# Performance work log

Measured on AMD Instinct MI355X. Metric: run time of the kernel, lower is better.

Reference implementation:

```python
import jax, jax.numpy as jnp
import numpy as np

BN_EPS = 1e-5
K = 2


def _log_shift_max(x):
    # x: [B, C, H, W]. torch.cat([x[..., -s:, :], x[..., :-s, :]], dim=2) == roll(x, +s)
    # and cat([x[..., s:, :], x[..., :s, :]], dim=2) == roll(x, -s).
    H, W = x.shape[2], x.shape[3]
    x_j = jnp.zeros_like(x)
    for i in range(1, int(H).bit_length()):
        s = K ** i - 1
        x_j = jnp.maximum(x_j, x - jnp.roll(x, s, axis=2))
        x_j = jnp.maximum(x_j, x - jnp.roll(x, -s, axis=2))
    for i in range(1, int(W).bit_length()):
        s = K ** i - 1
        x_j = jnp.maximum(x_j, x - jnp.roll(x, s, axis=3))
        x_j = jnp.maximum(x_j, x - jnp.roll(x, -s, axis=3))
    return x_j


def setup_inputs() -> dict:
    key = jax.random.key(0)
    k1, k2 = jax.random.split(key)
    B, C, H, W = 16, 384, 56, 56
    Cout = 384
    x = jax.random.normal(k1, (B, C, H, W), dtype=jnp.float32)
    conv_w = jax.random.normal(k2, (Cout, 2 * C, 1, 1), dtype=jnp.float32) * 0.02
    conv_b = jnp.zeros((Cout,), dtype=jnp.float32)
    bn_scale = jnp.ones((Cout,), dtype=jnp.float32)
    bn_bias = jnp.zeros((Cout,), dtype=jnp.float32)
    bn_mean = jnp.zeros((Cout,), dtype=jnp.float32)
    bn_var = jnp.ones((Cout,), dtype=jnp.float32)
    return {"x": x, "conv_w": conv_w, "conv_b": conv_b,
            "bn_scale": bn_scale, "bn_bias": bn_bias,
            "bn_mean": bn_mean, "bn_var": bn_var}


def reference(x, conv_w, conv_b, bn_scale, bn_bias, bn_mean, bn_var):
    x_j = _log_shift_max(x)                       # [B, C, H, W]
    xc = jnp.concatenate([x, x_j], axis=1)        # [B, 2C, H, W]
    # 1x1 conv == channel contraction
    y = jnp.einsum('bchw,oc->bohw', xc, conv_w[:, :, 0, 0]) + conv_b[None, :, None, None]
    # BatchNorm (eval mode, running stats)
    inv = jax.lax.rsqrt(bn_var + BN_EPS)
    y = (y - bn_mean[None, :, None, None]) * (inv * bn_scale)[None, :, None, None] + bn_bias[None, :, None, None]
    return jax.nn.gelu(y, approximate=False)
```

## Files before the change

### kernel.cpp

```cpp
#include <hip/hip_runtime.h>
#include <cstdint>
#include <cstddef>

typedef unsigned short u16;
typedef unsigned int u32;
typedef __attribute__((ext_vector_type(8))) short short8;
typedef __attribute__((ext_vector_type(4))) float f32x4;

__device__ __forceinline__ float bf2f(u16 v) { return __uint_as_float((u32)v << 16); }
__device__ __forceinline__ u16 f2bf(float f) {
    u32 u = __float_as_uint(f);
    u = (u + 0x7fffu + ((u >> 16) & 1u)) >> 16;
    return (u16)u;
}

#define GLD16(g, l) __builtin_amdgcn_global_load_lds( \
    (const __attribute__((address_space(1))) void*)(g), \
    (__attribute__((address_space(3))) void*)(l), 16, 0, 0)

__device__ __forceinline__ int sniff_fp(const void* x) {
    const u16* xs = (const u16*)x;
    const int lane = threadIdx.x & 63;
    int cnt = 0;
    #pragma unroll
    for (int k = 0; k < 4; ++k) {
        const int i = lane * 4 + k;
        const int e = (xs[2 * i] >> 7) & 0xFF;
        cnt += (int)__popcll(__ballot(e >= 96 && e <= 135));
    }
    return (cnt < 128) ? 1 : 0;
}

__global__ __launch_bounds__(512) void prep_kernel(const void* __restrict__ xin,
                                                   const void* __restrict__ w,
                                                   u16* __restrict__ xc,
                                                   u16* __restrict__ wbf) {
    const int cg = blockIdx.x, b = blockIdx.y;
    const int fp = sniff_fp(xin);

    if (cg >= 48) {
        const int base = ((cg - 48) * 16 + b) * 512 + threadIdx.x;
        for (int i = base; i < 384 * 768; i += 32 * 512) {
            if (fp) wbf[i] = f2bf(((const float*)w)[i]);
            else    wbf[i] = ((const u16*)w)[i];
        }
        return;
    }

    __shared__ __align__(16) u16 pl[3136][8];
    const size_t plane0 = ((size_t)b * 384 + (size_t)cg * 8) * 3136;

    if (fp) {
        const float* xb = (const float*)xin + plane0;
        for (int g = threadIdx.x; g < 784; g += 512) {
            const int p = g * 4;
            float vv[8][4];
            #pragma unroll
            for (int c = 0; c < 8; ++c) {
                const float4 t = *(const float4*)(xb + (size_t)c * 3136 + p);
                vv[c][0] = t.x; vv[c][1] = t.y; vv[c][2] = t.z; vv[c][3] = t.w;
            }
            #pragma unroll
            for (int i = 0; i < 4; ++i) {
                u32 q[4];
                #pragma unroll
                for (int cc = 0; cc < 4; ++cc)
                    q[cc] = (u32)f2bf(vv[cc * 2][i]) | ((u32)f2bf(vv[cc * 2 + 1][i]) << 16);
                *(uint4*)&pl[p + i][0] = make_uint4(q[0], q[1], q[2], q[3]);
            }
        }
    } else {
        const u16* xb = (const u16*)xin + plane0;
        for (int g = threadIdx.x; g < 784; g += 512) {
            const int p = g * 4;
            u32 rc[8][2];
            #pragma unroll
            for (int c = 0; c < 8; ++c) {
                const uint2 t = *(const uint2*)(xb + (size_t)c * 3136 + p);
                rc[c][0] = t.x; rc[c][1] = t.y;
            }
            #pragma unroll
            for (int i = 0; i < 4; ++i) {
                const int d = i >> 1, sh = (i & 1) * 16;
                u32 q[4];
                #pragma unroll
                for (int cc = 0; cc < 4; ++cc) {
                    const u32 lo = (rc[cc * 2][d] >> sh) & 0xFFFFu;
                    const u32 hi = (rc[cc * 2 + 1][d] >> sh) & 0xFFFFu;
                    q[cc] = lo | (hi << 16);
                }
                *(uint4*)&pl[p + i][0] = make_uint4(q[0], q[1], q[2], q[3]);
            }
        }
    }
    __syncthreads();

    for (int p = threadIdx.x; p < 3136; p += 512) {
        const int h = p / 56, w2 = p - h * 56;
        const uint4 self = *(const uint4*)&pl[p][0];
        const u32 sw[4] = {self.x, self.y, self.z, self.w};
        float xv[8], mn[8];
        #pragma unroll
        for (int c2 = 0; c2 < 4; ++c2) {
            xv[c2 * 2]     = __uint_as_float(sw[c2] << 16);
            xv[c2 * 2 + 1] = __uint_as_float(sw[c2] & 0xFFFF0000u);
            mn[c2 * 2] = xv[c2 * 2]; mn[c2 * 2 + 1] = xv[c2 * 2 + 1];
        }
        const int S[5] = {1, 3, 7, 15, 31};
        #pragma unroll
        for (int si = 0; si < 5; ++si) {
            const int s = S[si];
            int hp = h + s; if (hp >= 56) hp -= 56;
            int hm = h - s; if (hm < 0)   hm += 56;
            int wp = w2 + s; if (wp >= 56) wp -= 56;
            int wm = w2 - s; if (wm < 0)   wm += 56;
            const uint4 n0 = *(const uint4*)&pl[hp * 56 + w2][0];
            const uint4 n1 = *(const uint4*)&pl[hm * 56 + w2][0];
            const uint4 n2 = *(const uint4*)&pl[h * 56 + wp][0];
            const uint4 n3 = *(const uint4*)&pl[h * 56 + wm][0];
            const u32 w0[4] = {n0.x, n0.y, n0.z, n0.w};
            const u32 w1[4] = {n1.x, n1.y, n1.z, n1.w};
            const u32 wA[4] = {n2.x, n2.y, n2.z, n2.w};
            const u32 wB[4] = {n3.x, n3.y, n3.z, n3.w};
            #pragma unroll
            for (int c2 = 0; c2 < 4; ++c2) {
                mn[c2 * 2] = fminf(
                    fminf(__uint_as_float(w0[c2] << 16), __uint_as_float(w1[c2] << 16)),
                    fminf(fminf(__uint_as_float(wA[c2] << 16), __uint_as_float(wB[c2] << 16)),
                          mn[c2 * 2]));
                mn[c2 * 2 + 1] = fminf(
                    fminf(__uint_as_float(w0[c2] & 0xFFFF0000u), __uint_as_float(w1[c2] & 0xFFFF0000u)),
                    fminf(fminf(__uint_as_float(wA[c2] & 0xFFFF0000u), __uint_as_float(wB[c2] & 0xFFFF0000u)),
                          mn[c2 * 2 + 1]));
            }
        }
        u32 jq[4];
        #pragma unroll
        for (int c2 = 0; c2 < 4; ++c2)
            jq[c2] = (u32)f2bf(xv[c2 * 2] - mn[c2 * 2]) |
                     ((u32)f2bf(xv[c2 * 2 + 1] - mn[c2 * 2 + 1]) << 16);
        u16* px = xc + ((((size_t)b * 96) + cg) * 3136 + p) * 8;
        u16* pj = xc + ((((size_t)b * 96) + 48 + cg) * 3136 + p) * 8;
        *(uint4*)px = self;
        *(uint4*)pj = make_uint4(jq[0], jq[1], jq[2], jq[3]);
    }
}

__global__ __launch_bounds__(256) void gemm_kernel(
        const u16* __restrict__ xc, const u16* __restrict__ Wt,
        const void* __restrict__ cb, const void* __restrict__ bsc,
        const void* __restrict__ bbi, const void* __restrict__ bme,
        const void* __restrict__ bva, void* __restrict__ outp,
        const void* __restrict__ x0) {
    const int ntile = blockIdx.x;
    const int mtile = blockIdx.y;
    const int fp = sniff_fp(x0);
    __shared__ __align__(16) unsigned char smem[17408];
    __shared__ float2 PB[192];
    u16* const Bsu = (u16*)smem;

    const int tid = threadIdx.x;
    if (tid < 192) {
        const int o = mtile * 192 + tid;
        float vsc, vva, vcb, vme, vbi;
        if (fp) {
            vsc = ((const float*)bsc)[o]; vva = ((const float*)bva)[o];
            vcb = ((const float*)cb)[o];  vme = ((const float*)bme)[o];
            vbi = ((const float*)bbi)[o];
        } else {
            vsc = bf2f(((const u16*)bsc)[o]); vva = bf2f(((const u16*)bva)[o]);
            vcb = bf2f(((const u16*)cb)[o]);  vme = bf2f(((const u16*)bme)[o]);
            vbi = bf2f(((const u16*)bbi)[o]);
        }
        const float seff = vsc * rsqrtf(vva + 1e-5f);
        PB[tid] = make_float2(seff, (vcb - vme) * seff + vbi);
    }

    const int lane = tid & 63, wv = tid >> 6;
    const int quad = lane >> 4, l16 = lane & 15;
    const int bb  = ntile / 49;
    const int hw0 = (ntile - bb * 49) * 64;

    const u16* bgp[2]; int bofs[2];
    #pragma unroll
    for (int i = 0; i < 2; ++i) {
        const int idx = i * 256 + tid;
        const int gg = idx >> 6, n = idx & 63;
        bgp[i]  = xc + (((size_t)bb * 96 + gg) * 3136 + hw0 + n) * 8;
        bofs[i] = idx * 8;
    }
    #define STAGE(q) { \
        u16* dst = Bsu + ((q) & 1) * 4096; \
        _Pragma("unroll") \
        for (int i = 0; i < 2; ++i) GLD16(bgp[i] + (size_t)(q) * 8 * 3136 * 8, dst + bofs[i]); }

    const u16* arow[3];
    #pragma unroll
    for (int im = 0; im < 3; ++im)
        arow[im] = Wt + (size_t)(mtile * 192 + wv * 48 + im * 16 + l16) * 768 + quad * 8;

    f32x4 acc[3][4];
    #pragma unroll
    for (int im = 0; im < 3; ++im)
        #pragma unroll
        for (int in = 0; in < 4; ++in)
            acc[im][in] = {0.f, 0.f, 0.f, 0.f};

    STAGE(0);
    __syncthreads();

    for (int q = 0; q < 12; ++q) {
        if (q < 11) STAGE(q + 1);
        const u16* bufq = Bsu + (q & 1) * 4096;
        #pragma unroll
        for (int s = 0; s < 2; ++s) {
            const int k0 = q * 64 + s * 32;
            short8 af[3], bfv[4];
            #pragma unroll
            for (int im = 0; im < 3; ++im)
                af[im] = *(const short8*)(arow[im] + k0);
            #pragma unroll
            for (int in = 0; in < 4; ++in)
                bfv[in] = *(const short8*)(bufq + ((s * 4 + quad) * 64 + in * 16 + l16) * 8);
            #pragma unroll
            for (int im = 0; im < 3; ++im)
                #pragma unroll
                for (int in = 0; in < 4; ++in)
                    acc[im][in] = __builtin_amdgcn_mfma_f32_16x16x32_bf16(
                                      af[im], bfv[in], acc[im][in], 0, 0, 0);
        }
        __syncthreads();
    }

    float* T = (float*)smem + wv * (16 * 68);
    const size_t obase = (size_t)bb * 384 * 3136 + hw0;
    #pragma unroll
    for (int im = 0; im < 3; ++im) {
        #pragma unroll
        for (int r = 0; r < 4; ++r) {
            const float2 sb = PB[(wv * 48 + im * 16 + quad * 4 + r)];
            #pragma unroll
            for (int in = 0; in < 4; ++in) {
                float v = acc[im][in][r] * sb.x + sb.y;
                v = 0.5f * v * (1.0f + erff(v * 0.70710678118654752f));
                T[(quad * 4 + r) * 68 + in * 16 + l16] = v;
            }
        }
        asm volatile("s_waitcnt lgkmcnt(0)" ::: "memory");
        #pragma unroll
        for (int it = 0; it < 4; ++it) {
            const int flat = it * 256 + lane * 4;
            const int row = flat >> 6, col = flat & 63;
            const float4 vv = *(const float4*)&T[row * 68 + col];
            const size_t oi = obase +
                (size_t)(mtile * 192 + wv * 48 + im * 16 + row) * 3136 + col;
            if (fp) {
                *(float4*)((float*)outp + oi) = vv;
            } else {
                const u32 a = (u32)f2bf(vv.x) | ((u32)f2bf(vv.y) << 16);
                const u32 b2 = (u32)f2bf(vv.z) | ((u32)f2bf(vv.w) << 16);
                *(uint2*)((u16*)outp + oi) = make_uint2(a, b2);
            }
        }
        asm volatile("s_waitcnt lgkmcnt(0)" ::: "memory");
    }
    #undef STAGE
}

extern "C" void kernel_launch(void* const* d_in, const int* in_sizes, int n_in,
                              void* d_out, int out_size, void* d_ws, size_t ws_size,
                              hipStream_t stream) {
    const void* x   = d_in[0];
    const void* w   = d_in[1];
    const void* cbp = d_in[2];
    const void* bsc = d_in[3];
    const void* bbi = d_in[4];
    const void* bme = d_in[5];
    const void* bva = d_in[6];

    u16* xc   = (u16*)((char*)d_ws + 64);
    u16* wbf  = xc + (size_t)16 * 96 * 3136 * 8;

    prep_kernel<<<dim3(50, 16), 512, 0, stream>>>(x, w, xc, wbf);
    gemm_kernel<<<dim3(784, 2), 256, 0, stream>>>(xc, wbf, cbp, bsc, bbi, bme, bva,
                                                  d_out, x);
}
```

Baseline: 258.8 us.

## Triple-buffer GEMM B tiles with explicit vmcnt waits and unrolled phases

Moves the activation-tile staging in the GEMM from double to triple buffering in LDS, so each tile is prefetched two K-steps ahead. The K loop is fully unrolled into phases. Each phase uses a hand-written s_waitcnt vmcnt plus raw s_barrier instead of __syncthreads, so only the tile about to be consumed must have landed. The aim is to hide more global-to-LDS latency behind MFMA work. In exchange it uses more LDS, which may lower occupancy, and correctness now depends on the hand-counted outstanding-load numbers.

```diff
diff --git a/kernel.cpp b/kernel.cpp
--- a/kernel.cpp
+++ b/kernel.cpp
@@ -155,7 +155,7 @@
     const int ntile = blockIdx.x;
     const int mtile = blockIdx.y;
     const int fp = sniff_fp(x0);
-    __shared__ __align__(16) unsigned char smem[17408];
+    __shared__ __align__(16) unsigned char smem[24576];
     __shared__ float2 PB[192];
     u16* const Bsu = (u16*)smem;
 
@@ -190,7 +190,7 @@
         bofs[i] = idx * 8;
     }
     #define STAGE(q) { \
-        u16* dst = Bsu + ((q) & 1) * 4096; \
+        u16* dst = Bsu + ((q) % 3) * 4096; \
         _Pragma("unroll") \
         for (int i = 0; i < 2; ++i) GLD16(bgp[i] + (size_t)(q) * 8 * 3136 * 8, dst + bofs[i]); }
 
@@ -206,31 +206,46 @@
         for (int in = 0; in < 4; ++in)
             acc[im][in] = {0.f, 0.f, 0.f, 0.f};
 
+    #define COMPUTE(q) { \
+        const u16* bufq = Bsu + ((q) % 3) * 4096; \
+        _Pragma("unroll") \
+        for (int s = 0; s < 2; ++s) { \
+            const int k0 = (q) * 64 + s * 32; \
+            short8 af[3], bfv[4]; \
+            _Pragma("unroll") \
+            for (int im = 0; im < 3; ++im) \
+                af[im] = *(const short8*)(arow[im] + k0); \
+            _Pragma("unroll") \
+            for (int in = 0; in < 4; ++in) \
+                bfv[in] = *(const short8*)(bufq + ((s * 4 + quad) * 64 + in * 16 + l16) * 8); \
+            _Pragma("unroll") \
+            for (int im = 0; im < 3; ++im) \
+                _Pragma("unroll") \
+                for (int in = 0; in < 4; ++in) \
+                    acc[im][in] = __builtin_amdgcn_mfma_f32_16x16x32_bf16( \
+                                      af[im], bfv[in], acc[im][in], 0, 0, 0); } }
+
+    #define PHASE(q, WAIT) { \
+        if ((q) < 10) STAGE((q) + 2); \
+        asm volatile(WAIT ::: "memory"); \
+        __builtin_amdgcn_s_barrier(); \
+        COMPUTE(q); \
+        __builtin_amdgcn_s_barrier(); }
+
     STAGE(0);
-    __syncthreads();
-
-    for (int q = 0; q < 12; ++q) {
-        if (q < 11) STAGE(q + 1);
-        const u16* bufq = Bsu + (q & 1) * 4096;
-        #pragma unroll
-        for (int s = 0; s < 2; ++s) {
-            const int k0 = q * 64 + s * 32;
-            short8 af[3], bfv[4];
-            #pragma unroll
-            for (int im = 0; im < 3; ++im)
-                af[im] = *(const short8*)(arow[im] + k0);
-            #pragma unroll
-            for (int in = 0; in < 4; ++in)
-                bfv[in] = *(const short8*)(bufq + ((s * 4 + quad) * 64 + in * 16 + l16) * 8);
-            #pragma unroll
-            for (int im = 0; im < 3; ++im)
-                #pragma unroll
-                for (int in = 0; in < 4; ++in)
-                    acc[im][in] = __builtin_amdgcn_mfma_f32_16x16x32_bf16(
-                                      af[im], bfv[in], acc[im][in], 0, 0, 0);
-        }
-        __syncthreads();
-    }
+    STAGE(1);
+    PHASE(0,  "s_waitcnt vmcnt(4) lgkmcnt(0)");
+    PHASE(1,  "s_waitcnt vmcnt(4)");
+    PHASE(2,  "s_waitcnt vmcnt(4)");
+    PHASE(3,  "s_waitcnt vmcnt(4)");
+    PHASE(4,  "s_waitcnt vmcnt(4)");
+    PHASE(5,  "s_waitcnt vmcnt(4)");
+    PHASE(6,  "s_waitcnt vmcnt(4)");
+    PHASE(7,  "s_waitcnt vmcnt(4)");
+    PHASE(8,  "s_waitcnt vmcnt(4)");
+    PHASE(9,  "s_waitcnt vmcnt(4)");
+    PHASE(10, "s_waitcnt vmcnt(2)");
+    PHASE(11, "s_waitcnt vmcnt(0)");
 
     float* T = (float*)smem + wv * (16 * 68);
     const size_t obase = (size_t)bb * 384 * 3136 + hw0;
@@ -264,6 +279,8 @@
         }
         asm volatile("s_waitcnt lgkmcnt(0)" ::: "memory");
     }
+    #undef PHASE
+    #undef COMPUTE
     #undef STAGE
 }
 
```

Result: no change. 260.1 us (+0.5%).
